# Optimization experiments

Hardware: AMD Instinct MI355X
Metric: run time of the kernel (lower is better)

## Reference

```python
import jax, jax.numpy as jnp
import numpy as np

N_SEL = 8192
N_FEAT = 256
K_SUB = 256
N_PERS = 4
E_FULL = 262144
E_RAW = 262144
N_TOTAL = 8192
EPSILON = 0.5
LAMB1 = 0.5


def setup_inputs() -> dict:
    key = jax.random.key(0)
    ks = jax.random.split(key, 8)
    x = jax.random.normal(ks[0], (N_SEL, N_FEAT), dtype=jnp.float32)
    metric_weight = jax.random.uniform(ks[1], (N_PERS, N_FEAT), dtype=jnp.float32)
    selected_batch = jnp.sort(jax.random.randint(ks[2], (N_SEL,), 0, K_SUB, dtype=jnp.int32))
    selected_mapping = jax.random.randint(ks[3], (N_SEL,), 0, N_TOTAL, dtype=jnp.int32)
    selected_belong = jax.random.randint(ks[4], (K_SUB,), 0, K_SUB, dtype=jnp.int32)
    selected_score = jax.random.uniform(ks[5], (K_SUB,), dtype=jnp.float32)
    full_edge_index = jax.random.randint(ks[6], (2, E_FULL), 0, N_SEL, dtype=jnp.int32)
    raw_edge_index = jax.random.randint(ks[7], (2, E_RAW), 0, N_TOTAL, dtype=jnp.int32)
    return {"x": x, "metric_weight": metric_weight, "selected_batch": selected_batch,
            "selected_mapping": selected_mapping, "selected_belong": selected_belong,
            "selected_score": selected_score, "full_edge_index": full_edge_index,
            "raw_edge_index": raw_edge_index, "n_total": N_TOTAL}


def weighted_cosine(x, w):
    # x: [N, D], w: [P, D] -> mean over P perspectives of cosine sim
    h = x[None, :, :] * w[:, None, :]                        # [P, N, D]
    h = h / (jnp.linalg.norm(h, axis=-1, keepdims=True) + 1e-12)
    return jnp.einsum('pnd,pmd->nm', h, h) / w.shape[0]      # [N, N]


def reference(x, metric_weight, selected_batch, selected_mapping, selected_belong,
              selected_score, full_edge_index, raw_edge_index, n_total):
    n_sel = x.shape[0]
    k_sub = selected_score.shape[0]
    # scatter score normalization: scores of subgraphs sharing a 'belong' group sum to 1
    score_sum = jax.ops.segment_sum(selected_score, selected_belong, num_segments=k_sub)
    score = selected_score / score_sum[selected_belong]
    # z_node = x (no encoder); weighted-cosine metric over all selected nodes
    adj = weighted_cosine(x, metric_weight)                  # [N_sel, N_sel]
    # mask to allowed intra-subgraph edges (full_edge_index)
    mask = jnp.zeros_like(adj).at[full_edge_index[0], full_edge_index[1]].set(1.0)
    adj = adj * mask
    # postprocess: EpsilonNN threshold, then remove self loops
    adj = adj * (adj > EPSILON).astype(adj.dtype)
    diag = jnp.arange(n_sel)
    adj = adj.at[diag, diag].set(0.0)
    # per-edge weight = normalized score of the source node's subgraph, times lamb1
    adj_w = adj * (score[selected_batch] * LAMB1)[:, None]
    # map selected-node indices to global node ids and coalesce (sum duplicates)
    tmp = jnp.zeros((n_total, n_sel), adj.dtype).at[selected_mapping].add(adj_w)
    out = jnp.zeros((n_total, n_total), adj.dtype).at[:, selected_mapping].add(tmp)
    # add raw graph with weight (1 - lamb1); coalesce == dense scatter-add
    out = out.at[raw_edge_index[0], raw_edge_index[1]].add(1.0 - LAMB1)
    return out
```

## Files before the change

### kernel.cpp

```cpp
#include <hip/hip_runtime.h>

typedef float f4 __attribute__((ext_vector_type(4)));
typedef unsigned short us8 __attribute__((ext_vector_type(8)));

#define N_SEL   8192
#define N_FEAT  256
#define K_SUB   256
#define N_PERS  4
#define E_FULL  262144
#define E_RAW   262144
#define N_TOTAL 8192
#define EPSILON 0.5f
#define LAMB1   0.5f
#define ROW_CAP 128

#define WS_SCORE_OFF  (128 * 1024)
#define WS_CNT_OFF    (132 * 1024)
#define WS_FILL_OFF   (136 * 1024)
#define WS_XB_OFF     (256 * 1024)
#define WS_BUCKET_OFF (WS_XB_OFF + 4 * 1024 * 1024)
#define WS_LIST_OFF   (WS_BUCKET_OFF + 2 * 1024 * 1024)

#define B2F(s) __uint_as_float(((unsigned)(s)) << 16)

static __device__ __forceinline__ unsigned short f2b(float f) {
    unsigned u = __float_as_uint(f);
    unsigned r = u + 0x7FFFu + ((u >> 16) & 1u);
    return (unsigned short)(r >> 16);
}

__global__ __launch_bounds__(256) void prep_kernel(const f4* __restrict__ x4,
                                                   const f4* __restrict__ w4,
                                                   float* __restrict__ invn,
                                                   ushort4* __restrict__ xb,
                                                   const float* __restrict__ s,
                                                   const int* __restrict__ belong,
                                                   float* __restrict__ score,
                                                   int* __restrict__ row_fill,
                                                   int* __restrict__ cnt) {
    __shared__ float sv[K_SUB];
    __shared__ int bv[K_SUB];
    int gid = blockIdx.x * 256 + threadIdx.x;
    int wave = gid >> 6;
    int lane = threadIdx.x & 63;
    int n = wave >> 2;
    int p = wave & 3;
    f4 xv = x4[(size_t)n * 64 + lane];
    f4 wv = w4[p * 64 + lane];
    if (p == 0) {
        ushort4 b;
        b.x = f2b(xv.x); b.y = f2b(xv.y); b.z = f2b(xv.z); b.w = f2b(xv.w);
        xb[(size_t)n * 64 + lane] = b;
    }
    f4 h = xv * wv;
    float ss = h.x * h.x + h.y * h.y + h.z * h.z + h.w * h.w;
    #pragma unroll
    for (int off = 32; off; off >>= 1) ss += __shfl_xor(ss, off);
    if (lane == 0) invn[n * 4 + p] = 1.0f / (sqrtf(ss) + 1e-12f);

    if (gid < N_TOTAL) row_fill[gid] = 0;
    if (gid == 0) *cnt = 0;

    if (blockIdx.x == 0) {
        int t = threadIdx.x;
        sv[t] = s[t];
        bv[t] = belong[t];
        __syncthreads();
        int myb = bv[t];
        float sum = 0.0f;
        for (int k = 0; k < K_SUB; ++k)
            if (bv[k] == myb) sum += sv[k];
        score[t] = sv[t] / sum;
    }
}

__global__ __launch_bounds__(256) void bucket_kernel(const int* __restrict__ re,
                                                     int* __restrict__ row_fill,
                                                     unsigned short* __restrict__ bucket) {
    int t = blockIdx.x * 256 + threadIdx.x;
    if (t < E_RAW) {
        int u = re[t];
        int v = re[E_RAW + t];
        int pos = atomicAdd(&row_fill[u], 1);
        if (pos < ROW_CAP) bucket[u * ROW_CAP + pos] = (unsigned short)v;
    }
}

__global__ __launch_bounds__(256) void compose_kernel(f4* __restrict__ out4,
                                                      float* __restrict__ out,
                                                      const us8* __restrict__ xb8,
                                                      const f4* __restrict__ w4,
                                                      const int* __restrict__ fe,
                                                      const int* __restrict__ sel_batch,
                                                      const f4* __restrict__ invn4,
                                                      const float* __restrict__ score,
                                                      const int* __restrict__ row_fill,
                                                      const unsigned short* __restrict__ bucket,
                                                      int2* __restrict__ list,
                                                      int* __restrict__ cnt) {
    int b = blockIdx.x;
    int t = threadIdx.x;
    int lane = t & 63;
    int l16  = lane & 15;
    int g    = lane >> 4;
    int w    = t >> 6;

    size_t obase = (size_t)b * (N_TOTAL / 4);
    f4 z = (f4)0.0f;
    #pragma unroll
    for (int it = 0; it < 8; ++it)
        out4[obase + it * 256 + t] = z;

    float q0[16], q1[16], q2[16], q3[16];
    #pragma unroll
    for (int gg = 0; gg < 4; ++gg) {
        f4 w0 = w4[0 * 64 + l16 * 4 + gg];
        f4 w1 = w4[1 * 64 + l16 * 4 + gg];
        f4 w2 = w4[2 * 64 + l16 * 4 + gg];
        f4 w3 = w4[3 * 64 + l16 * 4 + gg];
        q0[gg*4+0]=w0.x*w0.x; q0[gg*4+1]=w0.y*w0.y; q0[gg*4+2]=w0.z*w0.z; q0[gg*4+3]=w0.w*w0.w;
        q1[gg*4+0]=w1.x*w1.x; q1[gg*4+1]=w1.y*w1.y; q1[gg*4+2]=w1.z*w1.z; q1[gg*4+3]=w1.w*w1.w;
        q2[gg*4+0]=w2.x*w2.x; q2[gg*4+1]=w2.y*w2.y; q2[gg*4+2]=w2.z*w2.z; q2[gg*4+3]=w2.w*w2.w;
        q3[gg*4+0]=w3.x*w3.x; q3[gg*4+1]=w3.y*w3.y; q3[gg*4+2]=w3.z*w3.z; q3[gg*4+3]=w3.w*w3.w;
    }

    int ebase = b * 32 + w * 8;
    #pragma unroll
    for (int it = 0; it < 2; ++it) {
        int e = ebase + it * 4 + g;
        int i = fe[e];
        int j = fe[E_FULL + e];
        const us8* ri = xb8 + (size_t)i * 32;
        const us8* rj = xb8 + (size_t)j * 32;
        us8 xi0 = ri[2 * l16], xi1 = ri[2 * l16 + 1];
        us8 xj0 = rj[2 * l16], xj1 = rj[2 * l16 + 1];

        float a0 = 0.f, a1 = 0.f, a2 = 0.f, a3 = 0.f;
        #pragma unroll
        for (int k = 0; k < 8; ++k) {
            float p0 = B2F(xi0[k]) * B2F(xj0[k]);
            float p1 = B2F(xi1[k]) * B2F(xj1[k]);
            a0 = fmaf(p1, q0[k + 8], fmaf(p0, q0[k], a0));
            a1 = fmaf(p1, q1[k + 8], fmaf(p0, q1[k], a1));
            a2 = fmaf(p1, q2[k + 8], fmaf(p0, q2[k], a2));
            a3 = fmaf(p1, q3[k + 8], fmaf(p0, q3[k], a3));
        }
        f4 ii = invn4[i];
        f4 ij = invn4[j];
        float v = a0 * (ii.x * ij.x) + a1 * (ii.y * ij.y) +
                  a2 * (ii.z * ij.z) + a3 * (ii.w * ij.w);
        v += __shfl_xor(v, 1);
        v += __shfl_xor(v, 2);
        v += __shfl_xor(v, 4);
        v += __shfl_xor(v, 8);

        if (l16 == 0 && i != j) {
            v *= 0.25f;
            if (v > EPSILON) {
                float val = v * score[sel_batch[i]] * LAMB1;
                int idx = atomicAdd(cnt, 1);
                int2 ent;
                ent.x = (i << 13) | j;
                ent.y = __float_as_int(val);
                list[idx] = ent;
            }
        }
    }

    __syncthreads();
    int rc = row_fill[b];
    if (rc > ROW_CAP) rc = ROW_CAP;
    const unsigned short* bk = bucket + b * ROW_CAP;
    for (int k = t; k < rc; k += 256)
        atomicAdd(&out[(size_t)b * N_TOTAL + bk[k]], 1.0f - LAMB1);
}

__global__ __launch_bounds__(256) void finalize_kernel(const int2* __restrict__ list,
                                                       const int* __restrict__ cnt,
                                                       const int* __restrict__ sel_map,
                                                       float* __restrict__ out) {
    int t = blockIdx.x * 256 + threadIdx.x;
    int n = *cnt;
    if (t >= n) return;
    int2 ek = list[t];
    for (int l = 0; l < t; ++l)
        if (list[l].x == ek.x) return;
    int i = ek.x >> 13;
    int j = ek.x & (N_SEL - 1);
    atomicAdd(&out[(size_t)sel_map[i] * N_TOTAL + sel_map[j]], __int_as_float(ek.y));
}

extern "C" void kernel_launch(void* const* d_in, const int* in_sizes, int n_in,
                              void* d_out, int out_size, void* d_ws, size_t ws_size,
                              hipStream_t stream) {
    const float* x         = (const float*)d_in[0];
    const float* mw        = (const float*)d_in[1];
    const int* sel_batch   = (const int*)d_in[2];
    const int* sel_map     = (const int*)d_in[3];
    const int* sel_belong  = (const int*)d_in[4];
    const float* sel_score = (const float*)d_in[5];
    const int* fe          = (const int*)d_in[6];
    const int* re          = (const int*)d_in[7];
    float* out             = (float*)d_out;

    char* ws        = (char*)d_ws;
    float* invn     = (float*)ws;
    float* score    = (float*)(ws + WS_SCORE_OFF);
    int* cnt        = (int*)(ws + WS_CNT_OFF);
    int* row_fill   = (int*)(ws + WS_FILL_OFF);
    ushort4* xb     = (ushort4*)(ws + WS_XB_OFF);
    unsigned short* bucket = (unsigned short*)(ws + WS_BUCKET_OFF);
    int2* list      = (int2*)(ws + WS_LIST_OFF);

    prep_kernel<<<8192, 256, 0, stream>>>(
        (const f4*)x, (const f4*)mw, invn, xb, sel_score, sel_belong, score,
        row_fill, cnt);
    bucket_kernel<<<E_RAW / 256, 256, 0, stream>>>(re, row_fill, bucket);
    compose_kernel<<<N_TOTAL, 256, 0, stream>>>(
        (f4*)out, out, (const us8*)xb, (const f4*)mw, fe, sel_batch,
        (const f4*)invn, score, row_fill, bucket, list, cnt);
    finalize_kernel<<<E_FULL / 256, 256, 0, stream>>>(list, cnt, sel_map, out);
}
```

Measured before the change: 109.7 us.

## Drop raw-edge bucketing, scatter raw edges directly, and batch edges per block

```diff
diff --git a/kernel.cpp b/kernel.cpp
--- a/kernel.cpp
+++ b/kernel.cpp
@@ -12,14 +12,11 @@
 #define N_TOTAL 8192
 #define EPSILON 0.5f
 #define LAMB1   0.5f
-#define ROW_CAP 128
 
 #define WS_SCORE_OFF  (128 * 1024)
 #define WS_CNT_OFF    (132 * 1024)
-#define WS_FILL_OFF   (136 * 1024)
 #define WS_XB_OFF     (256 * 1024)
-#define WS_BUCKET_OFF (WS_XB_OFF + 4 * 1024 * 1024)
-#define WS_LIST_OFF   (WS_BUCKET_OFF + 2 * 1024 * 1024)
+#define WS_LIST_OFF   (WS_XB_OFF + 4 * 1024 * 1024)
 
 #define B2F(s) __uint_as_float(((unsigned)(s)) << 16)
 
@@ -36,7 +33,6 @@
                                                    const float* __restrict__ s,
                                                    const int* __restrict__ belong,
                                                    float* __restrict__ score,
-                                                   int* __restrict__ row_fill,
                                                    int* __restrict__ cnt) {
     __shared__ float sv[K_SUB];
     __shared__ int bv[K_SUB];
@@ -58,7 +54,6 @@
     for (int off = 32; off; off >>= 1) ss += __shfl_xor(ss, off);
     if (lane == 0) invn[n * 4 + p] = 1.0f / (sqrtf(ss) + 1e-12f);
 
-    if (gid < N_TOTAL) row_fill[gid] = 0;
     if (gid == 0) *cnt = 0;
 
     if (blockIdx.x == 0) {
@@ -74,42 +69,24 @@
     }
 }
 
-__global__ __launch_bounds__(256) void bucket_kernel(const int* __restrict__ re,
-                                                     int* __restrict__ row_fill,
-                                                     unsigned short* __restrict__ bucket) {
-    int t = blockIdx.x * 256 + threadIdx.x;
-    if (t < E_RAW) {
-        int u = re[t];
-        int v = re[E_RAW + t];
-        int pos = atomicAdd(&row_fill[u], 1);
-        if (pos < ROW_CAP) bucket[u * ROW_CAP + pos] = (unsigned short)v;
-    }
-}
-
-__global__ __launch_bounds__(256) void compose_kernel(f4* __restrict__ out4,
-                                                      float* __restrict__ out,
-                                                      const us8* __restrict__ xb8,
-                                                      const f4* __restrict__ w4,
-                                                      const int* __restrict__ fe,
-                                                      const int* __restrict__ sel_batch,
-                                                      const f4* __restrict__ invn4,
-                                                      const float* __restrict__ score,
-                                                      const int* __restrict__ row_fill,
-                                                      const unsigned short* __restrict__ bucket,
-                                                      int2* __restrict__ list,
-                                                      int* __restrict__ cnt) {
+__global__ __launch_bounds__(256) void zero_edge_kernel(f4* __restrict__ out4,
+                                                        const us8* __restrict__ xb8,
+                                                        const f4* __restrict__ w4,
+                                                        const int* __restrict__ fe,
+                                                        const int* __restrict__ sel_batch,
+                                                        const f4* __restrict__ invn4,
+                                                        const float* __restrict__ score,
+                                                        int2* __restrict__ list,
+                                                        int* __restrict__ cnt) {
     int b = blockIdx.x;
     int t = threadIdx.x;
     int lane = t & 63;
     int l16  = lane & 15;
-    int g    = lane >> 4;
+    int sub  = lane >> 4;
     int w    = t >> 6;
 
-    size_t obase = (size_t)b * (N_TOTAL / 4);
-    f4 z = (f4)0.0f;
-    #pragma unroll
-    for (int it = 0; it < 8; ++it)
-        out4[obase + it * 256 + t] = z;
+    int ebase = b * 128 + w * 32;
+    int myidx = (lane < 32) ? fe[ebase + lane] : fe[E_FULL + ebase + (lane - 32)];
 
     float q0[16], q1[16], q2[16], q3[16];
     #pragma unroll
@@ -124,22 +101,38 @@
         q3[gg*4+0]=w3.x*w3.x; q3[gg*4+1]=w3.y*w3.y; q3[gg*4+2]=w3.z*w3.z; q3[gg*4+3]=w3.w*w3.w;
     }
 
-    int ebase = b * 32 + w * 8;
+    size_t obase = (size_t)b * 8192;
+    f4 z = (f4)0.0f;
+
+    int ci = __shfl(myidx, 0 + sub);
+    int cj = __shfl(myidx, 32 + 0 + sub);
+    const us8* ri = xb8 + (size_t)ci * 32;
+    const us8* rj = xb8 + (size_t)cj * 32;
+    us8 xi0 = ri[2 * l16], xi1 = ri[2 * l16 + 1];
+    us8 xj0 = rj[2 * l16], xj1 = rj[2 * l16 + 1];
+
     #pragma unroll
-    for (int it = 0; it < 2; ++it) {
-        int e = ebase + it * 4 + g;
-        int i = fe[e];
-        int j = fe[E_FULL + e];
-        const us8* ri = xb8 + (size_t)i * 32;
-        const us8* rj = xb8 + (size_t)j * 32;
-        us8 xi0 = ri[2 * l16], xi1 = ri[2 * l16 + 1];
-        us8 xj0 = rj[2 * l16], xj1 = rj[2 * l16 + 1];
+    for (int q = 0; q < 8; ++q) {
+        #pragma unroll
+        for (int k = 0; k < 4; ++k)
+            out4[obase + q * 1024 + k * 256 + t] = z;
+
+        int i = ci, j = cj;
+        us8 ai0 = xi0, ai1 = xi1, aj0 = xj0, aj1 = xj1;
+        if (q < 7) {
+            ci = __shfl(myidx, (q + 1) * 4 + sub);
+            cj = __shfl(myidx, 32 + (q + 1) * 4 + sub);
+            const us8* ri2 = xb8 + (size_t)ci * 32;
+            const us8* rj2 = xb8 + (size_t)cj * 32;
+            xi0 = ri2[2 * l16]; xi1 = ri2[2 * l16 + 1];
+            xj0 = rj2[2 * l16]; xj1 = rj2[2 * l16 + 1];
+        }
 
         float a0 = 0.f, a1 = 0.f, a2 = 0.f, a3 = 0.f;
         #pragma unroll
         for (int k = 0; k < 8; ++k) {
-            float p0 = B2F(xi0[k]) * B2F(xj0[k]);
-            float p1 = B2F(xi1[k]) * B2F(xj1[k]);
+            float p0 = B2F(ai0[k]) * B2F(aj0[k]);
+            float p1 = B2F(ai1[k]) * B2F(aj1[k]);
             a0 = fmaf(p1, q0[k + 8], fmaf(p0, q0[k], a0));
             a1 = fmaf(p1, q1[k + 8], fmaf(p0, q1[k], a1));
             a2 = fmaf(p1, q2[k + 8], fmaf(p0, q2[k], a2));
@@ -166,28 +159,32 @@
             }
         }
     }
-
-    __syncthreads();
-    int rc = row_fill[b];
-    if (rc > ROW_CAP) rc = ROW_CAP;
-    const unsigned short* bk = bucket + b * ROW_CAP;
-    for (int k = t; k < rc; k += 256)
-        atomicAdd(&out[(size_t)b * N_TOTAL + bk[k]], 1.0f - LAMB1);
-}
-
-__global__ __launch_bounds__(256) void finalize_kernel(const int2* __restrict__ list,
-                                                       const int* __restrict__ cnt,
-                                                       const int* __restrict__ sel_map,
-                                                       float* __restrict__ out) {
+}
+
+__global__ __launch_bounds__(256) void raw_finalize_kernel(const int* __restrict__ re,
+                                                           const int2* __restrict__ list,
+                                                           const int* __restrict__ cnt,
+                                                           const int* __restrict__ sel_map,
+                                                           float* __restrict__ out) {
     int t = blockIdx.x * 256 + threadIdx.x;
+    if (t < E_RAW) {
+        int u = re[t];
+        int v = re[E_RAW + t];
+        atomicAdd(&out[(size_t)u * N_TOTAL + v], 1.0f - LAMB1);
+    }
     int n = *cnt;
-    if (t >= n) return;
-    int2 ek = list[t];
-    for (int l = 0; l < t; ++l)
-        if (list[l].x == ek.x) return;
-    int i = ek.x >> 13;
-    int j = ek.x & (N_SEL - 1);
-    atomicAdd(&out[(size_t)sel_map[i] * N_TOTAL + sel_map[j]], __int_as_float(ek.y));
+    if (t < n) {
+        int2 ek = list[t];
+        bool first = true;
+        for (int l = 0; l < t; ++l)
+            if (list[l].x == ek.x) { first = false; break; }
+        if (first) {
+            int i = ek.x >> 13;
+            int j = ek.x & (N_SEL - 1);
+            atomicAdd(&out[(size_t)sel_map[i] * N_TOTAL + sel_map[j]],
+                      __int_as_float(ek.y));
+        }
+    }
 }
 
 extern "C" void kernel_launch(void* const* d_in, const int* in_sizes, int n_in,
@@ -203,21 +200,17 @@
     const int* re          = (const int*)d_in[7];
     float* out             = (float*)d_out;
 
-    char* ws        = (char*)d_ws;
-    float* invn     = (float*)ws;
-    float* score    = (float*)(ws + WS_SCORE_OFF);
-    int* cnt        = (int*)(ws + WS_CNT_OFF);
-    int* row_fill   = (int*)(ws + WS_FILL_OFF);
-    ushort4* xb     = (ushort4*)(ws + WS_XB_OFF);
-    unsigned short* bucket = (unsigned short*)(ws + WS_BUCKET_OFF);
-    int2* list      = (int2*)(ws + WS_LIST_OFF);
+    char* ws       = (char*)d_ws;
+    float* invn    = (float*)ws;
+    float* score   = (float*)(ws + WS_SCORE_OFF);
+    int* cnt       = (int*)(ws + WS_CNT_OFF);
+    ushort4* xb    = (ushort4*)(ws + WS_XB_OFF);
+    int2* list     = (int2*)(ws + WS_LIST_OFF);
 
     prep_kernel<<<8192, 256, 0, stream>>>(
-        (const f4*)x, (const f4*)mw, invn, xb, sel_score, sel_belong, score,
-        row_fill, cnt);
-    bucket_kernel<<<E_RAW / 256, 256, 0, stream>>>(re, row_fill, bucket);
-    compose_kernel<<<N_TOTAL, 256, 0, stream>>>(
-        (f4*)out, out, (const us8*)xb, (const f4*)mw, fe, sel_batch,
-        (const f4*)invn, score, row_fill, bucket, list, cnt);
-    finalize_kernel<<<E_FULL / 256, 256, 0, stream>>>(list, cnt, sel_map, out);
-}
+        (const f4*)x, (const f4*)mw, invn, xb, sel_score, sel_belong, score, cnt);
+    zero_edge_kernel<<<2048, 256, 0, stream>>>(
+        (f4*)out, (const us8*)xb, (const f4*)mw, fe, sel_batch,
+        (const f4*)invn, score, list, cnt);
+    raw_finalize_kernel<<<1024, 256, 0, stream>>>(re, list, cnt, sel_map, out);
+}
```

After: 97.63 us. 1.12x faster.
